# Performance work log

Measured on AMD Instinct MI355X. Metric: run time of the kernel, lower is better.

Reference implementation:

```python
import jax, jax.numpy as jnp
import numpy as np

EMBED_DIM = 1024
NUM_HEADS = 16
HEAD_DIM = EMBED_DIM // NUM_HEADS


def setup_inputs() -> dict:
    key = jax.random.key(0)
    ks = jax.random.split(key, 6)
    s = 1.0 / np.sqrt(EMBED_DIM)
    x = jax.random.normal(ks[0], (2, 2048, EMBED_DIM), dtype=jnp.float32)
    Wk = jax.random.uniform(ks[1], (EMBED_DIM, EMBED_DIM), jnp.float32, -s, s)
    Wq = jax.random.uniform(ks[2], (EMBED_DIM, EMBED_DIM), jnp.float32, -s, s)
    Wv = jax.random.uniform(ks[3], (EMBED_DIM, EMBED_DIM), jnp.float32, -s, s)
    Wo = jax.random.uniform(ks[4], (EMBED_DIM, EMBED_DIM), jnp.float32, -s, s)
    bo = jax.random.uniform(ks[5], (EMBED_DIM,), jnp.float32, -s, s)
    return {"x": x, "Wq": Wq, "Wk": Wk, "Wv": Wv, "Wo": Wo, "bo": bo}


def reference(x, Wq, Wk, Wv, Wo, bo):
    b, s, e = x.shape
    h, d = NUM_HEADS, HEAD_DIM
    scale = d ** (-0.5)
    # nn.Linear: y = x @ W.T ; here W stored as [out, in] -> use W.T
    q = (x @ Wq.T).reshape(b, s, h, d).transpose(0, 2, 1, 3)  # b h s d
    k = (x @ Wk.T).reshape(b, s, h, d).transpose(0, 2, 1, 3)
    v = (x @ Wv.T).reshape(b, s, h, d).transpose(0, 2, 1, 3)
    logits = jnp.einsum('bhqd,bhkd->bhqk', q, k) * scale
    attn = jax.nn.softmax(logits, axis=-1)
    out = jnp.einsum('bhqk,bhkd->bhqd', attn, v)
    out = out.transpose(0, 2, 1, 3).reshape(b, s, e)
    return out @ Wo.T + bo
```

## Files before the change

kernel.cpp:

```cpp
#include <hip/hip_runtime.h>
#include <hip/hip_bf16.h>

using short8 = __attribute__((ext_vector_type(8))) short;
using f32x4  = __attribute__((ext_vector_type(4))) float;

#if __has_builtin(__builtin_amdgcn_exp2f)
#define EXP2(x) __builtin_amdgcn_exp2f(x)
#else
#define EXP2(x) exp2f(x)
#endif

__device__ __forceinline__ short f2bf(float f) {
    union { float f; unsigned u; } v; v.f = f;
    unsigned r = v.u + 0x7fffu + ((v.u >> 16) & 1u);
    return (short)(r >> 16);
}
__device__ __forceinline__ unsigned pack_trunc(float a, float b) {
    union { float f; unsigned u; } ua, ub; ua.f = a; ub.f = b;
#if __has_builtin(__builtin_amdgcn_perm)
    return __builtin_amdgcn_perm(ub.u, ua.u, 0x07060302u);
#else
    return (ub.u & 0xFFFF0000u) | (ua.u >> 16);
#endif
}
__device__ __forceinline__ void async_copy16(const short* g, short* s) {
    __builtin_amdgcn_global_load_lds(
        (const __attribute__((address_space(1))) void*)g,
        (__attribute__((address_space(3))) void*)s, 16, 0, 0);
}

__global__ __launch_bounds__(256) void cvt_f32_bf16(
    const float* __restrict__ s0, const float* __restrict__ s1,
    const float* __restrict__ s2, const float* __restrict__ s3,
    const float* __restrict__ s4,
    short* __restrict__ d0, short* __restrict__ d1, short* __restrict__ d2,
    short* __restrict__ d3, short* __restrict__ d4,
    int n0, int n1, int n2, int n3, int n4) {
    const float* s; short* d; int n;
    switch (blockIdx.y) {
        case 0: s = s0; d = d0; n = n0; break;
        case 1: s = s1; d = d1; n = n1; break;
        case 2: s = s2; d = d2; n = n2; break;
        case 3: s = s3; d = d3; n = n3; break;
        default: s = s4; d = d4; n = n4; break;
    }
    const int idx = (blockIdx.x * 256 + threadIdx.x) * 4;
    if (idx < n) {
        float4 v = *(const float4*)(s + idx);
        short4 o;
        o.x = f2bf(v.x); o.y = f2bf(v.y); o.z = f2bf(v.z); o.w = f2bf(v.w);
        *(short4*)(d + idx) = o;
    }
}

template <int MODE, typename OT>
__device__ __forceinline__ void gemm_body(const short* __restrict__ A,
                                          const short* __restrict__ B,
                                          OT* __restrict__ C,
                                          const float* __restrict__ bias,
                                          float scale) {
    constexpr int Kd = 1024, Nd = 1024, Sd = 2048;
    __shared__ __align__(16) short As[128 * 32];
    __shared__ __align__(16) short Bs[128 * 32];

    const int tid  = threadIdx.x;
    const int w    = tid >> 6, lane = tid & 63;
    const int quad = lane >> 4, l16 = lane & 15;
    const int wm   = (w >> 1) * 64, wn = (w & 1) * 64;
    const int bm   = blockIdx.y * 128, bn = blockIdx.x * 128;

    f32x4 acc[4][4];
#pragma unroll
    for (int i = 0; i < 4; ++i)
#pragma unroll
        for (int j = 0; j < 4; ++j) acc[i][j] = (f32x4){0.f, 0.f, 0.f, 0.f};

    for (int k0 = 0; k0 < Kd; k0 += 32) {
        __syncthreads();
#pragma unroll
        for (int c = 0; c < 2; ++c) {
            int li  = c * 256 + tid;
            int row = li >> 2;
            int col = (li & 3) * 8;
            async_copy16(A + (size_t)(bm + row) * Kd + k0 + col, &As[li * 8]);
            async_copy16(B + (size_t)(bn + row) * Kd + k0 + col, &Bs[li * 8]);
        }
        __syncthreads();

        short8 af[4], bfv[4];
#pragma unroll
        for (int mi = 0; mi < 4; ++mi)
            af[mi] = *(const short8*)(&As[(wm + mi * 16 + l16) * 32 + quad * 8]);
#pragma unroll
        for (int ni = 0; ni < 4; ++ni)
            bfv[ni] = *(const short8*)(&Bs[(wn + ni * 16 + l16) * 32 + quad * 8]);
#pragma unroll
        for (int mi = 0; mi < 4; ++mi)
#pragma unroll
            for (int ni = 0; ni < 4; ++ni) {
                if constexpr (MODE == 2)
                    acc[mi][ni] = __builtin_amdgcn_mfma_f32_16x16x32_bf16(
                        bfv[ni], af[mi], acc[mi][ni], 0, 0, 0);
                else
                    acc[mi][ni] = __builtin_amdgcn_mfma_f32_16x16x32_bf16(
                        af[mi], bfv[ni], acc[mi][ni], 0, 0, 0);
            }
    }

    if constexpr (MODE == 2) {
#pragma unroll
        for (int mi = 0; mi < 4; ++mi) {
            const int m_g = bm + wm + mi * 16 + l16;
            const int b_  = m_g >> 11, s_ = m_g & 2047;
#pragma unroll
            for (int ni = 0; ni < 4; ++ni)
#pragma unroll
                for (int r = 0; r < 4; ++r) {
                    const int n_g = bn + wn + ni * 16 + quad * 4 + r;
                    C[(size_t)b_ * Nd * Sd + (size_t)n_g * Sd + s_] =
                        f2bf(acc[mi][ni][r]);
                }
        }
    } else {
#pragma unroll
        for (int ni = 0; ni < 4; ++ni) {
            const int colg = bn + wn + ni * 16 + l16;
            const float bv = (MODE == 1 && bias) ? bias[colg] : 0.f;
#pragma unroll
            for (int mi = 0; mi < 4; ++mi)
#pragma unroll
                for (int r = 0; r < 4; ++r) {
                    const int rowg = bm + wm + mi * 16 + quad * 4 + r;
                    if constexpr (MODE == 0)
                        C[(size_t)rowg * Nd + colg] = f2bf(acc[mi][ni][r] * scale);
                    else
                        C[(size_t)rowg * Nd + colg] = acc[mi][ni][r] + bv;
                }
        }
    }
}

#define CSC 0.18033688f

__global__ __launch_bounds__(256, 2) void proj_gemm(
    const short* __restrict__ X,
    const short* __restrict__ Wq, const short* __restrict__ Wk,
    const short* __restrict__ Wv,
    short* __restrict__ Qo, short* __restrict__ Ko, short* __restrict__ VTo) {
    if (blockIdx.z == 0)
        gemm_body<0, short>(X, Wq, Qo, nullptr, CSC);
    else if (blockIdx.z == 1)
        gemm_body<0, short>(X, Wk, Ko, nullptr, 1.0f);
    else
        gemm_body<2, short>(X, Wv, VTo, nullptr, 1.0f);
}

__global__ __launch_bounds__(256, 2) void out_gemm(
    const short* __restrict__ A, const short* __restrict__ W,
    const float* __restrict__ bias, float* __restrict__ C) {
    gemm_body<1, float>(A, W, C, bias, 1.0f);
}

__global__ __launch_bounds__(256, 2) void attn_kernel(
    const short* __restrict__ Q, const short* __restrict__ K,
    const short* __restrict__ VT, short* __restrict__ O) {
    constexpr int S = 2048, E = 1024;
    __shared__ __align__(16) short Ks[64 * 64];
    __shared__ __align__(16) short Vs[64 * 64];
    __shared__ __align__(16) short Pt[4 * 16 * 80];

    const int tid  = threadIdx.x;
    const int w    = tid >> 6, lane = tid & 63;
    const int quad = lane >> 4, l16 = lane & 15;
    const int bh   = blockIdx.y, b = bh >> 4, h = bh & 15;
    const int qt   = blockIdx.x;

    const int    q0   = qt * 64 + w * 16;
    const size_t base = (size_t)b * S * E;
    const size_t vtb  = (size_t)b * E * S;
    const int    hc   = h * 64;

    short8 aq[2];
    {
        const short* qp = Q + base + (size_t)(q0 + l16) * E + hc + quad * 8;
        aq[0] = *(const short8*)(qp);
        aq[1] = *(const short8*)(qp + 32);
    }

    f32x4 oT[4], o_sum = (f32x4){0.f, 0.f, 0.f, 0.f};
#pragma unroll
    for (int i = 0; i < 4; ++i) oT[i] = (f32x4){0.f, 0.f, 0.f, 0.f};

    int          sdst[2];
    const short* kga[2];
    const short* vga[2];
#pragma unroll
    for (int c = 0; c < 2; ++c) {
        int li = c * 256 + tid, row = li >> 3, cc = li & 7;
        sdst[c] = row * 64 + ((cc ^ (row & 7)) * 8);
        kga[c]  = K + base + (size_t)row * E + hc + cc * 8;
        vga[c]  = VT + vtb + (size_t)(hc + row) * S + cc * 8;
    }

    short8 kr[2], vr[2];
#pragma unroll
    for (int c = 0; c < 2; ++c) {
        kr[c] = *(const short8*)(kga[c]);
        vr[c] = *(const short8*)(vga[c]);
    }

    const short8 ones = (short8){0x3F80, 0x3F80, 0x3F80, 0x3F80,
                                 0x3F80, 0x3F80, 0x3F80, 0x3F80};
    const float  LB   = 0.00281502f;
    short*       Ptw  = &Pt[w * 16 * 80];
    const int    xr   = l16 & 7;

    for (int kt = 0; kt < S / 64; ++kt) {
        __syncthreads();
#pragma unroll
        for (int c = 0; c < 2; ++c) {
            *(short8*)(&Ks[sdst[c]]) = kr[c];
            *(short8*)(&Vs[sdst[c]]) = vr[c];
        }
        __syncthreads();

        if (kt + 1 < S / 64) {
#pragma unroll
            for (int c = 0; c < 2; ++c) {
                kr[c] = *(const short8*)(kga[c] + (size_t)(kt + 1) * 64 * E);
                vr[c] = *(const short8*)(vga[c] + (kt + 1) * 64);
            }
        }

#pragma unroll
        for (int kn = 0; kn < 4; ++kn) {
            const short* kb  = &Ks[(kn * 16 + l16) * 64];
            short8       bk0 = *(const short8*)(kb + ((quad ^ xr) * 8));
            short8       bk1 = *(const short8*)(kb + (((quad + 4) ^ xr) * 8));
            f32x4 a = (f32x4){LB, LB, LB, LB};
            a = __builtin_amdgcn_mfma_f32_16x16x32_bf16(bk0, aq[0], a, 0, 0, 0);
            a = __builtin_amdgcn_mfma_f32_16x16x32_bf16(bk1, aq[1], a, 0, 0, 0);
            float e0 = EXP2(a[0]), e1 = EXP2(a[1]);
            float e2 = EXP2(a[2]), e3 = EXP2(a[3]);
            uint2 pk;
            pk.x = pack_trunc(e0, e1);
            pk.y = pack_trunc(e2, e3);
            *(uint2*)(&Ptw[l16 * 80 + kn * 16 + quad * 4]) = pk;
        }

#pragma unroll
        for (int ks = 0; ks < 2; ++ks) {
            short8 pf = *(const short8*)(&Ptw[l16 * 80 + ks * 32 + quad * 8]);
            o_sum = __builtin_amdgcn_mfma_f32_16x16x32_bf16(ones, pf, o_sum, 0, 0, 0);
#pragma unroll
            for (int ni = 0; ni < 4; ++ni) {
                const int rv = ni * 16 + l16;
                short8 vb =
                    *(const short8*)(&Vs[rv * 64 + (((ks * 4 + quad) ^ (rv & 7)) * 8)]);
                oT[ni] = __builtin_amdgcn_mfma_f32_16x16x32_bf16(
                    vb, pf, oT[ni], 0, 0, 0);
            }
        }
    }

    const float inv = 1.0f / o_sum[0];
    const int   qg  = q0 + l16;
#pragma unroll
    for (int ni = 0; ni < 4; ++ni) {
        short4 ov;
        ov.x = f2bf(oT[ni][0] * inv);
        ov.y = f2bf(oT[ni][1] * inv);
        ov.z = f2bf(oT[ni][2] * inv);
        ov.w = f2bf(oT[ni][3] * inv);
        *(short4*)(&O[base + (size_t)qg * E + hc + ni * 16 + quad * 4]) = ov;
    }
}

extern "C" void kernel_launch(void* const* d_in, const int* in_sizes, int n_in,
                              void* d_out, int out_size, void* d_ws, size_t ws_size,
                              hipStream_t stream) {
    const float* x  = (const float*)d_in[0];
    const float* Wq = (const float*)d_in[1];
    const float* Wk = (const float*)d_in[2];
    const float* Wv = (const float*)d_in[3];
    const float* Wo = (const float*)d_in[4];
    const float* bo = (const float*)d_in[5];
    float* out = (float*)d_out;

    constexpr int XN = 2 * 2048 * 1024;
    constexpr int WN = 1024 * 1024;

    short* Xb  = (short*)d_ws;
    short* Wqb = Xb + XN;
    short* Wkb = Wqb + WN;
    short* Wvb = Wkb + WN;
    short* Wob = Wvb + WN;
    short* Qb  = Wob + WN;
    short* Kb  = Qb + XN;
    short* VTb = Kb + XN;

    cvt_f32_bf16<<<dim3(4096, 5), 256, 0, stream>>>(
        x, Wq, Wk, Wv, Wo, Xb, Wqb, Wkb, Wvb, Wob, XN, WN, WN, WN, WN);
    proj_gemm<<<dim3(8, 32, 3), 256, 0, stream>>>(Xb, Wqb, Wkb, Wvb, Qb, Kb, VTb);
    attn_kernel<<<dim3(32, 32), 256, 0, stream>>>(Qb, Kb, VTb, Xb );
    out_gemm<<<dim3(8, 32, 1), 256, 0, stream>>>(Xb, Wob, bo, out);
}
```

Measured before the change: 193.8 us.

## Process two query groups per wave in attention and narrow out-GEMM tiles

The attention kernel now handles 32 query rows per wave (128 per block), so each K/V tile loaded into shared memory and each V fragment read serves two MFMA query groups. This halves the attention grid and the K/V global and LDS traffic per query, at the cost of more registers and a larger P scratch buffer. The output GEMM becomes a dedicated kernel with 128x64 tiles, doubling its block count to 512 to spread work across more CUs. It also drops the generic bias/float path from the shared GEMM body.

Result: faster. 187.3 us (-3.4%).

```diff
diff --git a/kernel.cpp b/kernel.cpp
--- a/kernel.cpp
+++ b/kernel.cpp
@@ -53,11 +53,10 @@
     }
 }
 
-template <int MODE, typename OT>
+template <int MODE>
 __device__ __forceinline__ void gemm_body(const short* __restrict__ A,
                                           const short* __restrict__ B,
-                                          OT* __restrict__ C,
-                                          const float* __restrict__ bias,
+                                          short* __restrict__ C,
                                           float scale) {
     constexpr int Kd = 1024, Nd = 1024, Sd = 2048;
     __shared__ __align__(16) short As[128 * 32];
@@ -125,16 +124,12 @@
 #pragma unroll
         for (int ni = 0; ni < 4; ++ni) {
             const int colg = bn + wn + ni * 16 + l16;
-            const float bv = (MODE == 1 && bias) ? bias[colg] : 0.f;
 #pragma unroll
             for (int mi = 0; mi < 4; ++mi)
 #pragma unroll
                 for (int r = 0; r < 4; ++r) {
                     const int rowg = bm + wm + mi * 16 + quad * 4 + r;
-                    if constexpr (MODE == 0)
-                        C[(size_t)rowg * Nd + colg] = f2bf(acc[mi][ni][r] * scale);
-                    else
-                        C[(size_t)rowg * Nd + colg] = acc[mi][ni][r] + bv;
+                    C[(size_t)rowg * Nd + colg] = f2bf(acc[mi][ni][r] * scale);
                 }
         }
     }
@@ -148,17 +143,74 @@
     const short* __restrict__ Wv,
     short* __restrict__ Qo, short* __restrict__ Ko, short* __restrict__ VTo) {
     if (blockIdx.z == 0)
-        gemm_body<0, short>(X, Wq, Qo, nullptr, CSC);
+        gemm_body<0>(X, Wq, Qo, CSC);
     else if (blockIdx.z == 1)
-        gemm_body<0, short>(X, Wk, Ko, nullptr, 1.0f);
+        gemm_body<0>(X, Wk, Ko, 1.0f);
     else
-        gemm_body<2, short>(X, Wv, VTo, nullptr, 1.0f);
+        gemm_body<2>(X, Wv, VTo, 1.0f);
 }
 
 __global__ __launch_bounds__(256, 2) void out_gemm(
-    const short* __restrict__ A, const short* __restrict__ W,
+    const short* __restrict__ A, const short* __restrict__ B,
     const float* __restrict__ bias, float* __restrict__ C) {
-    gemm_body<1, float>(A, W, C, bias, 1.0f);
+    constexpr int Kd = 1024, Nd = 1024;
+    __shared__ __align__(16) short As[128 * 32];
+    __shared__ __align__(16) short Bs[64 * 32];
+
+    const int tid  = threadIdx.x;
+    const int w    = tid >> 6, lane = tid & 63;
+    const int quad = lane >> 4, l16 = lane & 15;
+    const int wm   = (w >> 1) * 64, wn = (w & 1) * 32;
+    const int bm   = blockIdx.y * 128, bn = blockIdx.x * 64;
+
+    f32x4 acc[4][2];
+#pragma unroll
+    for (int i = 0; i < 4; ++i)
+#pragma unroll
+        for (int j = 0; j < 2; ++j) acc[i][j] = (f32x4){0.f, 0.f, 0.f, 0.f};
+
+    for (int k0 = 0; k0 < Kd; k0 += 32) {
+        __syncthreads();
+#pragma unroll
+        for (int c = 0; c < 2; ++c) {
+            int li  = c * 256 + tid;
+            int row = li >> 2;
+            int col = (li & 3) * 8;
+            async_copy16(A + (size_t)(bm + row) * Kd + k0 + col, &As[li * 8]);
+        }
+        {
+            int row = tid >> 2, col = (tid & 3) * 8;
+            async_copy16(B + (size_t)(bn + row) * Kd + k0 + col, &Bs[tid * 8]);
+        }
+        __syncthreads();
+
+        short8 af[4], bfv[2];
+#pragma unroll
+        for (int mi = 0; mi < 4; ++mi)
+            af[mi] = *(const short8*)(&As[(wm + mi * 16 + l16) * 32 + quad * 8]);
+#pragma unroll
+        for (int ni = 0; ni < 2; ++ni)
+            bfv[ni] = *(const short8*)(&Bs[(wn + ni * 16 + l16) * 32 + quad * 8]);
+#pragma unroll
+        for (int mi = 0; mi < 4; ++mi)
+#pragma unroll
+            for (int ni = 0; ni < 2; ++ni)
+                acc[mi][ni] = __builtin_amdgcn_mfma_f32_16x16x32_bf16(
+                    af[mi], bfv[ni], acc[mi][ni], 0, 0, 0);
+    }
+
+#pragma unroll
+    for (int ni = 0; ni < 2; ++ni) {
+        const int colg = bn + wn + ni * 16 + l16;
+        const float bv = bias[colg];
+#pragma unroll
+        for (int mi = 0; mi < 4; ++mi)
+#pragma unroll
+            for (int r = 0; r < 4; ++r) {
+                const int rowg = bm + wm + mi * 16 + quad * 4 + r;
+                C[(size_t)rowg * Nd + colg] = acc[mi][ni][r] + bv;
+            }
+    }
 }
 
 __global__ __launch_bounds__(256, 2) void attn_kernel(
@@ -167,7 +219,7 @@
     constexpr int S = 2048, E = 1024;
     __shared__ __align__(16) short Ks[64 * 64];
     __shared__ __align__(16) short Vs[64 * 64];
-    __shared__ __align__(16) short Pt[4 * 16 * 80];
+    __shared__ __align__(16) short Pt[4 * 32 * 72];
 
     const int tid  = threadIdx.x;
     const int w    = tid >> 6, lane = tid & 63;
@@ -175,21 +227,26 @@
     const int bh   = blockIdx.y, b = bh >> 4, h = bh & 15;
     const int qt   = blockIdx.x;
 
-    const int    q0   = qt * 64 + w * 16;
+    const int    q0   = qt * 128 + w * 32;
     const size_t base = (size_t)b * S * E;
     const size_t vtb  = (size_t)b * E * S;
     const int    hc   = h * 64;
 
-    short8 aq[2];
-    {
-        const short* qp = Q + base + (size_t)(q0 + l16) * E + hc + quad * 8;
-        aq[0] = *(const short8*)(qp);
-        aq[1] = *(const short8*)(qp + 32);
-    }
-
-    f32x4 oT[4], o_sum = (f32x4){0.f, 0.f, 0.f, 0.f};
-#pragma unroll
-    for (int i = 0; i < 4; ++i) oT[i] = (f32x4){0.f, 0.f, 0.f, 0.f};
+    short8 aq[2][2];
+#pragma unroll
+    for (int qg = 0; qg < 2; ++qg) {
+        const short* qp = Q + base + (size_t)(q0 + qg * 16 + l16) * E + hc + quad * 8;
+        aq[qg][0] = *(const short8*)(qp);
+        aq[qg][1] = *(const short8*)(qp + 32);
+    }
+
+    f32x4 oT[2][4], o_sum[2];
+#pragma unroll
+    for (int qg = 0; qg < 2; ++qg) {
+        o_sum[qg] = (f32x4){0.f, 0.f, 0.f, 0.f};
+#pragma unroll
+        for (int i = 0; i < 4; ++i) oT[qg][i] = (f32x4){0.f, 0.f, 0.f, 0.f};
+    }
 
     int          sdst[2];
     const short* kga[2];
@@ -212,7 +269,7 @@
     const short8 ones = (short8){0x3F80, 0x3F80, 0x3F80, 0x3F80,
                                  0x3F80, 0x3F80, 0x3F80, 0x3F80};
     const float  LB   = 0.00281502f;
-    short*       Ptw  = &Pt[w * 16 * 80];
+    short*       Ptw  = &Pt[w * 32 * 72];
     const int    xr   = l16 & 7;
 
     for (int kt = 0; kt < S / 64; ++kt) {
@@ -237,42 +294,56 @@
             const short* kb  = &Ks[(kn * 16 + l16) * 64];
             short8       bk0 = *(const short8*)(kb + ((quad ^ xr) * 8));
             short8       bk1 = *(const short8*)(kb + (((quad + 4) ^ xr) * 8));
-            f32x4 a = (f32x4){LB, LB, LB, LB};
-            a = __builtin_amdgcn_mfma_f32_16x16x32_bf16(bk0, aq[0], a, 0, 0, 0);
-            a = __builtin_amdgcn_mfma_f32_16x16x32_bf16(bk1, aq[1], a, 0, 0, 0);
-            float e0 = EXP2(a[0]), e1 = EXP2(a[1]);
-            float e2 = EXP2(a[2]), e3 = EXP2(a[3]);
-            uint2 pk;
-            pk.x = pack_trunc(e0, e1);
-            pk.y = pack_trunc(e2, e3);
-            *(uint2*)(&Ptw[l16 * 80 + kn * 16 + quad * 4]) = pk;
+#pragma unroll
+            for (int qg = 0; qg < 2; ++qg) {
+                f32x4 a = (f32x4){LB, LB, LB, LB};
+                a = __builtin_amdgcn_mfma_f32_16x16x32_bf16(bk0, aq[qg][0], a, 0, 0, 0);
+                a = __builtin_amdgcn_mfma_f32_16x16x32_bf16(bk1, aq[qg][1], a, 0, 0, 0);
+                float e0 = EXP2(a[0]), e1 = EXP2(a[1]);
+                float e2 = EXP2(a[2]), e3 = EXP2(a[3]);
+                uint2 pk;
+                pk.x = pack_trunc(e0, e1);
+                pk.y = pack_trunc(e2, e3);
+                *(uint2*)(&Ptw[(qg * 16 + l16) * 72 + kn * 16 + quad * 4]) = pk;
+            }
         }
 
 #pragma unroll
         for (int ks = 0; ks < 2; ++ks) {
-            short8 pf = *(const short8*)(&Ptw[l16 * 80 + ks * 32 + quad * 8]);
-            o_sum = __builtin_amdgcn_mfma_f32_16x16x32_bf16(ones, pf, o_sum, 0, 0, 0);
+            short8 pf[2];
+#pragma unroll
+            for (int qg = 0; qg < 2; ++qg) {
+                pf[qg] = *(const short8*)(
+                    &Ptw[(qg * 16 + l16) * 72 + ks * 32 + quad * 8]);
+                o_sum[qg] = __builtin_amdgcn_mfma_f32_16x16x32_bf16(
+                    ones, pf[qg], o_sum[qg], 0, 0, 0);
+            }
 #pragma unroll
             for (int ni = 0; ni < 4; ++ni) {
                 const int rv = ni * 16 + l16;
                 short8 vb =
                     *(const short8*)(&Vs[rv * 64 + (((ks * 4 + quad) ^ (rv & 7)) * 8)]);
-                oT[ni] = __builtin_amdgcn_mfma_f32_16x16x32_bf16(
-                    vb, pf, oT[ni], 0, 0, 0);
-            }
-        }
-    }
-
-    const float inv = 1.0f / o_sum[0];
-    const int   qg  = q0 + l16;
-#pragma unroll
-    for (int ni = 0; ni < 4; ++ni) {
-        short4 ov;
-        ov.x = f2bf(oT[ni][0] * inv);
-        ov.y = f2bf(oT[ni][1] * inv);
-        ov.z = f2bf(oT[ni][2] * inv);
-        ov.w = f2bf(oT[ni][3] * inv);
-        *(short4*)(&O[base + (size_t)qg * E + hc + ni * 16 + quad * 4]) = ov;
+#pragma unroll
+                for (int qg = 0; qg < 2; ++qg)
+                    oT[qg][ni] = __builtin_amdgcn_mfma_f32_16x16x32_bf16(
+                        vb, pf[qg], oT[qg][ni], 0, 0, 0);
+            }
+        }
+    }
+
+#pragma unroll
+    for (int qg = 0; qg < 2; ++qg) {
+        const float inv = 1.0f / o_sum[qg][0];
+        const int   qg_ = q0 + qg * 16 + l16;
+#pragma unroll
+        for (int ni = 0; ni < 4; ++ni) {
+            short4 ov;
+            ov.x = f2bf(oT[qg][ni][0] * inv);
+            ov.y = f2bf(oT[qg][ni][1] * inv);
+            ov.z = f2bf(oT[qg][ni][2] * inv);
+            ov.w = f2bf(oT[qg][ni][3] * inv);
+            *(short4*)(&O[base + (size_t)qg_ * E + hc + ni * 16 + quad * 4]) = ov;
+        }
     }
 }
 
@@ -302,6 +373,6 @@
     cvt_f32_bf16<<<dim3(4096, 5), 256, 0, stream>>>(
         x, Wq, Wk, Wv, Wo, Xb, Wqb, Wkb, Wvb, Wob, XN, WN, WN, WN, WN);
     proj_gemm<<<dim3(8, 32, 3), 256, 0, stream>>>(Xb, Wqb, Wkb, Wvb, Qb, Kb, VTb);
-    attn_kernel<<<dim3(32, 32), 256, 0, stream>>>(Qb, Kb, VTb, Xb );
-    out_gemm<<<dim3(8, 32, 1), 256, 0, stream>>>(Xb, Wob, bo, out);
-}
+    attn_kernel<<<dim3(16, 32), 256, 0, stream>>>(Qb, Kb, VTb, Xb );
+    out_gemm<<<dim3(16, 32), 256, 0, stream>>>(Xb, Wob, bo, out);
+}
```
